# Performance work log

Measured on AMD Instinct MI355X. Metric: run time of the kernel, lower is better.

The kernel has to match this reference:

```python
import jax, jax.numpy as jnp
import numpy as np

K = 3            # context window size
VOCAB = 50257
EMBED = 1024
SEQ = 2048
BATCH = 2


def setup_inputs() -> dict:
    key = jax.random.key(0)
    ks = jax.random.split(key, 8)
    tokens_seq = jax.random.randint(ks[0], (SEQ, BATCH), 0, VOCAB, dtype=jnp.int64)
    s = 0.02
    E = jax.random.normal(ks[1], (VOCAB, EMBED), dtype=jnp.float32) * s
    W1 = jax.random.normal(ks[2], (K * EMBED, EMBED), dtype=jnp.float32) * s
    b1 = jnp.zeros((EMBED,), dtype=jnp.float32)
    W2 = jax.random.normal(ks[3], (EMBED, EMBED), dtype=jnp.float32) * s
    b2 = jnp.zeros((EMBED,), dtype=jnp.float32)
    Wout = jax.random.normal(ks[4], (EMBED, VOCAB), dtype=jnp.float32) * s
    bout = jnp.zeros((VOCAB,), dtype=jnp.float32)
    return {"tokens_seq": tokens_seq, "E": E, "W1": W1, "b1": b1,
            "W2": W2, "b2": b2, "Wout": Wout, "bout": bout}


def reference(tokens_seq, E, W1, b1, W2, b2, Wout, bout):
    S, B = tokens_seq.shape
    # pad with k-1 zero-token rows at the front, then take length-k windows
    pad = jnp.zeros((K - 1, B), dtype=tokens_seq.dtype)
    padded = jnp.concatenate([pad, tokens_seq], axis=0)          # (S+K-1, B)
    # windows[t, b, i] = padded[t+i, b]  (same as torch unfold + permute)
    windows = jnp.stack([padded[i:i + S] for i in range(K)], axis=-1)  # (S, B, K)
    emb = E[windows]                                              # (S, B, K, EMBED)
    x = emb.reshape(S, B, K * EMBED)                              # concat of k embeddings
    h = jax.nn.silu(jnp.einsum('sbi,io->sbo', x, W1) + b1)
    h = jax.nn.silu(jnp.einsum('sbi,io->sbo', h, W2) + b2)
    logits = jnp.einsum('sbi,iv->sbv', h, Wout) + bout            # (S, B, VOCAB)
    return logits
```

## Files before the change

kernel.cpp:

```cpp
#include <hip/hip_runtime.h>
#include <hip/hip_bf16.h>

#define SEQ    2048
#define BATCH  2
#define MROWS  (SEQ*BATCH)
#define EMBED  1024
#define KCTX   3
#define XDIM   (KCTX*EMBED)
#define VOCAB  50257
#define VPAD2  50432
#define GK     1024
#define NBLKN  197
#define NWG    (16*NBLKN)

using u16 = unsigned short;
typedef __attribute__((ext_vector_type(8))) short   frag_ab;
typedef __attribute__((ext_vector_type(4))) float   frag_cd;

__device__ __forceinline__ u16 f2bf(float f) {
  union { float f; unsigned u; } v; v.f = f;
  unsigned r = v.u + 0x7fffu + ((v.u >> 16) & 1u);
  return (u16)(r >> 16);
}

__device__ __forceinline__ void gload16(const u16* g, const u16* l) {
  __builtin_amdgcn_global_load_lds((const __attribute__((address_space(1))) void*)g,
                                   (__attribute__((address_space(3))) void*)l, 16, 0, 0);
}

__global__ void gather_x(const int* __restrict__ tokens,
                         const float* __restrict__ E,
                         u16* __restrict__ XB) {
  const int r = blockIdx.x;
  const int s = r >> 1, b = r & 1;
  #pragma unroll
  for (int i = 0; i < KCTX; ++i) {
    int t = s + i - (KCTX - 1);
    int tok = (t >= 0) ? tokens[t * BATCH + b] : 0;
    const float* src = &E[(size_t)tok * EMBED];
    u16* dst = &XB[(size_t)r * XDIM + i * EMBED];
    int c = threadIdx.x * 4;
    float4 v = *(const float4*)&src[c];
    u16 o[4] = { f2bf(v.x), f2bf(v.y), f2bf(v.z), f2bf(v.w) };
    *(ulong1*)&dst[c] = *(ulong1*)o;
  }
}

__global__ void transpose_cvt(const float* __restrict__ W,
                              u16* __restrict__ WT,
                              int K, int N) {
  __shared__ float tile[32][33];
  const int nb = blockIdx.x * 32, kb = blockIdx.y * 32;
  const int tx = threadIdx.x & 31, ty = threadIdx.x >> 5;
  #pragma unroll
  for (int i = 0; i < 32; i += 8) {
    int k = kb + ty + i, n = nb + tx;
    tile[ty + i][tx] = (n < N) ? W[(size_t)k * N + n] : 0.f;
  }
  __syncthreads();
  #pragma unroll
  for (int i = 0; i < 32; i += 8) {
    int n = nb + ty + i, k = kb + tx;
    WT[(size_t)n * K + k] = f2bf(tile[tx][ty + i]);
  }
}

template<int EPI>
__global__ __launch_bounds__(256, 2)
void gemm_bt(const u16* __restrict__ A, const u16* __restrict__ BT,
             const float* __restrict__ bias, void* __restrict__ Cout,
             int K, int Nout) {
  __shared__ u16 lA[128 * 64];
  __shared__ u16 lB[128 * 64];
  const int tid  = threadIdx.x;
  const int wave = tid >> 6, lane = tid & 63;
  const int m0 = blockIdx.y * 128;
  const int n0 = blockIdx.x * 128;
  const int wm = (wave >> 1) * 64;
  const int wn = (wave & 1) * 64;

  frag_cd acc[4][4];
  #pragma unroll
  for (int i = 0; i < 4; ++i)
    #pragma unroll
    for (int j = 0; j < 4; ++j)
      acc[i][j] = (frag_cd)0.f;

  const int srow = lane >> 3;
  const int skc  = ((lane & 7) ^ srow) * 8;

  for (int k0 = 0; k0 < K; k0 += 64) {
    #pragma unroll
    for (int i = 0; i < 4; ++i) {
      int chunk = wave * 4 + i;
      int r = chunk * 8 + srow;
      const u16* ga = &A [(size_t)(m0 + r) * K + k0 + skc];
      const u16* gb = &BT[(size_t)(n0 + r) * K + k0 + skc];
      gload16(ga, &lA[chunk * 512 + lane * 8]);
      gload16(gb, &lB[chunk * 512 + lane * 8]);
    }
    __syncthreads();

    #pragma unroll
    for (int kk = 0; kk < 2; ++kk) {
      const int c15 = lane & 15;
      const int s   = kk * 4 + (lane >> 4);
      const int ko  = (s ^ (c15 & 7)) * 8;
      frag_ab af[4], bfr[4];
      #pragma unroll
      for (int i = 0; i < 4; ++i) {
        af[i]  = *(const frag_ab*)&lA[(wm + i * 16 + c15) * 64 + ko];
        bfr[i] = *(const frag_ab*)&lB[(wn + i * 16 + c15) * 64 + ko];
      }
      #pragma unroll
      for (int i = 0; i < 4; ++i)
        #pragma unroll
        for (int j = 0; j < 4; ++j)
          acc[i][j] = __builtin_amdgcn_mfma_f32_16x16x32_bf16(
              af[i], bfr[j], acc[i][j], 0, 0, 0);
    }
    __syncthreads();
  }

  const int cr = (lane >> 4) * 4;
  const int cc = lane & 15;
  if (EPI == 0) {
    u16* H = (u16*)Cout;
    #pragma unroll
    for (int j = 0; j < 4; ++j) {
      int colg = n0 + wn + j * 16 + cc;
      float bv = bias[colg];
      #pragma unroll
      for (int i = 0; i < 4; ++i)
        #pragma unroll
        for (int t = 0; t < 4; ++t) {
          int rowg = m0 + wm + i * 16 + cr + t;
          float v = acc[i][j][t] + bv;
          v = v / (1.f + __expf(-v));
          H[(size_t)rowg * Nout + colg] = f2bf(v);
        }
    }
  } else {
    float* O = (float*)Cout;
    #pragma unroll
    for (int j = 0; j < 4; ++j) {
      int colg = n0 + wn + j * 16 + cc;
      if (colg < Nout) {
        float bv = bias[colg];
        #pragma unroll
        for (int i = 0; i < 4; ++i)
          #pragma unroll
          for (int t = 0; t < 4; ++t) {
            int rowg = m0 + wm + i * 16 + cr + t;
            O[(size_t)rowg * Nout + colg] = acc[i][j][t] + bv;
          }
      }
    }
  }
}

#define BARR   asm volatile("s_barrier" ::: "memory")
#define VMCNT4 asm volatile("s_waitcnt vmcnt(4)" ::: "memory")
#define LGKM0  asm volatile("s_waitcnt lgkmcnt(0)" ::: "memory")
#define SCHED0 __builtin_amdgcn_sched_barrier(0)
#define PRIO1  __builtin_amdgcn_s_setprio(1)
#define PRIO0  __builtin_amdgcn_s_setprio(0)

#define DSREAD(DST, AREG, IMM) \
  asm volatile("ds_read_b128 %0, %1 offset:%2" : "=v"(DST) : "v"(AREG), "i"(IMM))

#define ADV { pa0 += 32; pa1 += 32; pb0 += 32; pb1 += 32; }

#define KT(REGH, REGW, HIMM, WIMM, WP) { \
  VMCNT4; BARR; \
  gload16(pa0, (const u16*)(smraw + (WP)         + stoff)); \
  gload16(pa1, (const u16*)(smraw + (WP) +  8192 + stoff)); \
  gload16(pb0, (const u16*)(smraw + (WP) + 16384 + stoff)); \
  gload16(pb1, (const u16*)(smraw + (WP) + 24576 + stoff)); \
  ADV; \
  DSREAD(wF[0], REGW, (WIMM) + 0*1024); \
  DSREAD(wF[1], REGW, (WIMM) + 1*1024); \
  DSREAD(wF[2], REGW, (WIMM) + 2*1024); \
  DSREAD(wF[3], REGW, (WIMM) + 3*1024); \
  DSREAD(hF[0], REGH, (HIMM) + 0*1024); \
  DSREAD(hF[1], REGH, (HIMM) + 1*1024); \
  DSREAD(hF[2], REGH, (HIMM) + 2*1024); \
  DSREAD(hF[3], REGH, (HIMM) + 3*1024); \
  DSREAD(hF[4], REGH, (HIMM) + 4*1024); \
  DSREAD(hF[5], REGH, (HIMM) + 5*1024); \
  DSREAD(hF[6], REGH, (HIMM) + 6*1024); \
  DSREAD(hF[7], REGH, (HIMM) + 7*1024); \
  LGKM0; SCHED0; \
  PRIO1; \
  _Pragma("unroll") for (int nf = 0; nf < 4; ++nf) \
  _Pragma("unroll") for (int mf = 0; mf < 8; ++mf) \
    acc[mf][nf] = __builtin_amdgcn_mfma_f32_16x16x32_bf16(hF[mf], wF[nf], acc[mf][nf], 0, 0, 0); \
  PRIO0; SCHED0; }

__global__ __launch_bounds__(512, 2)
void gemm256(const u16* __restrict__ A, const u16* __restrict__ BT,
             const float* __restrict__ bias, float* __restrict__ O) {
  extern __shared__ char smraw[];

  const int bid = blockIdx.x;
  const int wg  = (bid & 7) * (NWG / 8) + (bid >> 3);
  const int m0  = (wg & 15) * 256;
  const int n0  = (wg >> 4) * 256;

  const int tid  = threadIdx.x;
  const int lane = tid & 63, wave = tid >> 6;
  const int wm = wave >> 2, wn = wave & 3;

  const int stoff = wave * 1024 + lane * 16;
  const int srow  = wave * 16 + (lane >> 2);
  const int ke    = ((lane & 3) ^ ((lane >> 3) & 3)) * 8;

  const u16* pa0 = A + (size_t)(m0 + srow      ) * GK + ke;
  const u16* pa1 = A + (size_t)(m0 + srow + 128) * GK + ke;
  const u16* pb0 = BT + (size_t)(n0 + srow      ) * GK + ke;
  const u16* pb1 = BT + (size_t)(n0 + srow + 128) * GK + ke;

  const unsigned dynbase = (unsigned)(size_t)(__attribute__((address_space(3))) char*)smraw;
  const int c = lane & 15, q = lane >> 4;
  const unsigned swq  = ((unsigned)q << 4) ^ (((unsigned)(c >> 1) & 3u) << 4);
  const unsigned regH_lo = dynbase + (unsigned)((wm * 128 + c) * 64) + swq;
  const unsigned regW_lo = dynbase + 16384u + (unsigned)((wn * 64 + c) * 64) + swq;
  const unsigned regH_hi = regH_lo + 65536u;
  const unsigned regW_hi = regW_lo + 65536u;

  frag_ab hF[8], wF[4];
  frag_cd acc[8][4];
  #pragma unroll
  for (int i = 0; i < 8; ++i)
    #pragma unroll
    for (int j = 0; j < 4; ++j)
      acc[i][j] = (frag_cd)0.f;

  gload16(pa0, (const u16*)(smraw +     0 + stoff));
  gload16(pa1, (const u16*)(smraw +  8192 + stoff));
  gload16(pb0, (const u16*)(smraw + 16384 + stoff));
  gload16(pb1, (const u16*)(smraw + 24576 + stoff));
  ADV;
  gload16(pa0, (const u16*)(smraw + 32768 +     0 + stoff));
  gload16(pa1, (const u16*)(smraw + 32768 +  8192 + stoff));
  gload16(pb0, (const u16*)(smraw + 32768 + 16384 + stoff));
  gload16(pb1, (const u16*)(smraw + 32768 + 24576 + stoff));
  ADV;

  #pragma unroll 1
  for (int tt = 0; tt < 10; ++tt) {
    KT(regH_lo, regW_lo,     0,     0, 65536);
    KT(regH_lo, regW_lo, 32768, 32768,     0);
    KT(regH_hi, regW_hi,     0,     0, 32768);
  }
  KT(regH_lo, regW_lo,     0,     0, 65536);
  KT(regH_lo, regW_lo, 32768, 32768,     0);

  asm volatile("s_waitcnt vmcnt(0) lgkmcnt(0)" ::: "memory");
  BARR;

  float* lfs = (float*)smraw;
  const int colg = n0 + wn * 64 + c * 4;
  #pragma unroll
  for (int mf = 0; mf < 8; ++mf) {
    const int lbase = wave * 1088 + (mf & 1) * 8704;
    #pragma unroll
    for (int nf = 0; nf < 4; ++nf)
      #pragma unroll
      for (int t = 0; t < 4; ++t)
        lfs[lbase + (q * 4 + t) * 68 + nf * 16 + c] = acc[mf][nf][t];
    #pragma unroll
    for (int p = 0; p < 4; ++p) {
      frag_cd v = *(const frag_cd*)&lfs[lbase + (p * 4 + q) * 68 + c * 4];
      const int rowg = m0 + wm * 128 + mf * 16 + p * 4 + q;
      if (colg + 3 < VOCAB) {
        frag_cd bv = *(const frag_cd*)&bias[colg];
        v += bv;
        *(frag_cd*)&O[(size_t)rowg * VOCAB + colg] = v;
      } else {
        #pragma unroll
        for (int t = 0; t < 4; ++t)
          if (colg + t < VOCAB)
            O[(size_t)rowg * VOCAB + colg + t] = v[t] + bias[colg + t];
      }
    }
  }
}

extern "C" void kernel_launch(void* const* d_in, const int* in_sizes, int n_in,
                              void* d_out, int out_size, void* d_ws, size_t ws_size,
                              hipStream_t stream) {
  const int*   tokens = (const int*)  d_in[0];
  const float* E      = (const float*)d_in[1];
  const float* W1     = (const float*)d_in[2];
  const float* b1     = (const float*)d_in[3];
  const float* W2     = (const float*)d_in[4];
  const float* b2     = (const float*)d_in[5];
  const float* Wout   = (const float*)d_in[6];
  const float* bout   = (const float*)d_in[7];
  float* out = (float*)d_out;

  char* p = (char*)d_ws;
  u16* XB  = (u16*)p; p += (size_t)MROWS * XDIM  * 2;
  u16* WOT = (u16*)p; p += (size_t)VPAD2 * EMBED * 2;
  u16* H1  = (u16*)p; p += (size_t)MROWS * EMBED * 2;
  u16* H2  = (u16*)p; p += (size_t)MROWS * EMBED * 2;
  u16* W1T = (u16*)p; p += (size_t)EMBED * XDIM  * 2;
  u16* W2T = (u16*)p; p += (size_t)EMBED * EMBED * 2;

  hipFuncSetAttribute((const void*)gemm256,
                      hipFuncAttributeMaxDynamicSharedMemorySize, 98304);

  gather_x<<<MROWS, 256, 0, stream>>>(tokens, E, XB);
  transpose_cvt<<<dim3(EMBED/32, XDIM/32),  256, 0, stream>>>(W1,   W1T, XDIM,  EMBED);
  transpose_cvt<<<dim3(EMBED/32, EMBED/32), 256, 0, stream>>>(W2,   W2T, EMBED, EMBED);
  transpose_cvt<<<dim3(VPAD2/32, EMBED/32), 256, 0, stream>>>(Wout, WOT, EMBED, VOCAB);

  gemm_bt<0><<<dim3(EMBED/128, MROWS/128), 256, 0, stream>>>(XB, W1T, b1, H1, XDIM,  EMBED);
  gemm_bt<0><<<dim3(EMBED/128, MROWS/128), 256, 0, stream>>>(H1, W2T, b2, H2, EMBED, EMBED);

  gemm256<<<NWG, 512, 98304, stream>>>(H2, WOT, bout, out);
}
```

Baseline: 796.5 us.

## Restructure vocab GEMM to BK=64 double-buffered pipeline with interleaved LDS waits

The output-projection GEMM changes from a triple-buffered K=32 pipeline to a double-buffered K=64 one, using 64 KB LDS stages, a new XOR swizzle and a reworked global-to-LDS load mapping. Each window waits for all outstanding global loads, issues the next stage's prefetch, then runs two 32-wide K halves. Within each half, MFMAs are split into per-row groups gated by decreasing lgkmcnt waits, so compute can start before every LDS read has returned. The aim is fewer barriers and better overlap of ds_reads with MFMA. The cost is a full vmcnt(0) wait per window, only one stage of prefetch lookahead, and a larger LDS footprint of 128 KB.

```diff
diff --git a/kernel.cpp b/kernel.cpp
--- a/kernel.cpp
+++ b/kernel.cpp
@@ -160,46 +160,65 @@
 }
 
 #define BARR   asm volatile("s_barrier" ::: "memory")
-#define VMCNT4 asm volatile("s_waitcnt vmcnt(4)" ::: "memory")
-#define LGKM0  asm volatile("s_waitcnt lgkmcnt(0)" ::: "memory")
+#define VMCNT0 asm volatile("s_waitcnt vmcnt(0)" ::: "memory")
+#define LGKMC(N) asm volatile("s_waitcnt lgkmcnt(" #N ")" ::: "memory")
 #define SCHED0 __builtin_amdgcn_sched_barrier(0)
 #define PRIO1  __builtin_amdgcn_s_setprio(1)
 #define PRIO0  __builtin_amdgcn_s_setprio(0)
-
 #define DSREAD(DST, AREG, IMM) \
   asm volatile("ds_read_b128 %0, %1 offset:%2" : "=v"(DST) : "v"(AREG), "i"(IMM))
-
-#define ADV { pa0 += 32; pa1 += 32; pb0 += 32; pb1 += 32; }
-
-#define KT(REGH, REGW, HIMM, WIMM, WP) { \
-  VMCNT4; BARR; \
-  gload16(pa0, (const u16*)(smraw + (WP)         + stoff)); \
-  gload16(pa1, (const u16*)(smraw + (WP) +  8192 + stoff)); \
-  gload16(pb0, (const u16*)(smraw + (WP) + 16384 + stoff)); \
-  gload16(pb1, (const u16*)(smraw + (WP) + 24576 + stoff)); \
-  ADV; \
-  DSREAD(wF[0], REGW, (WIMM) + 0*1024); \
-  DSREAD(wF[1], REGW, (WIMM) + 1*1024); \
-  DSREAD(wF[2], REGW, (WIMM) + 2*1024); \
-  DSREAD(wF[3], REGW, (WIMM) + 3*1024); \
-  DSREAD(hF[0], REGH, (HIMM) + 0*1024); \
-  DSREAD(hF[1], REGH, (HIMM) + 1*1024); \
-  DSREAD(hF[2], REGH, (HIMM) + 2*1024); \
-  DSREAD(hF[3], REGH, (HIMM) + 3*1024); \
-  DSREAD(hF[4], REGH, (HIMM) + 4*1024); \
-  DSREAD(hF[5], REGH, (HIMM) + 5*1024); \
-  DSREAD(hF[6], REGH, (HIMM) + 6*1024); \
-  DSREAD(hF[7], REGH, (HIMM) + 7*1024); \
-  LGKM0; SCHED0; \
+#define MFMA4(MF) { \
+  _Pragma("unroll") for (int nf = 0; nf < 4; ++nf) \
+    acc[MF][nf] = __builtin_amdgcn_mfma_f32_16x16x32_bf16(hF[MF], wF[nf], acc[MF][nf], 0, 0, 0); }
+
+#define BSTAGE(WP) { \
+  gload16(pa,          (const u16*)(smraw + (WP)         + stoffB)); \
+  gload16(pa +  65536, (const u16*)(smraw + (WP) +  8192 + stoffB)); \
+  gload16(pa + 131072, (const u16*)(smraw + (WP) + 16384 + stoffB)); \
+  gload16(pa + 196608, (const u16*)(smraw + (WP) + 24576 + stoffB)); \
+  gload16(pb,          (const u16*)(smraw + (WP) + 32768 + stoffB)); \
+  gload16(pb +  65536, (const u16*)(smraw + (WP) + 40960 + stoffB)); \
+  gload16(pb + 131072, (const u16*)(smraw + (WP) + 49152 + stoffB)); \
+  gload16(pb + 196608, (const u16*)(smraw + (WP) + 57344 + stoffB)); \
+  pa += 64; pb += 64; }
+
+#define BRD(REGW, REGH) { \
+  DSREAD(wF[0], REGW, 0*2048); \
+  DSREAD(wF[1], REGW, 1*2048); \
+  DSREAD(wF[2], REGW, 2*2048); \
+  DSREAD(wF[3], REGW, 3*2048); \
+  DSREAD(hF[0], REGH, 0*2048); \
+  DSREAD(hF[1], REGH, 1*2048); \
+  DSREAD(hF[2], REGH, 2*2048); \
+  DSREAD(hF[3], REGH, 3*2048); \
+  DSREAD(hF[4], REGH, 4*2048); \
+  DSREAD(hF[5], REGH, 5*2048); \
+  DSREAD(hF[6], REGH, 6*2048); \
+  DSREAD(hF[7], REGH, 7*2048); }
+
+#define GROUPS8 { \
   PRIO1; \
-  _Pragma("unroll") for (int nf = 0; nf < 4; ++nf) \
-  _Pragma("unroll") for (int mf = 0; mf < 8; ++mf) \
-    acc[mf][nf] = __builtin_amdgcn_mfma_f32_16x16x32_bf16(hF[mf], wF[nf], acc[mf][nf], 0, 0, 0); \
+  LGKMC(7); SCHED0; MFMA4(0); \
+  LGKMC(6); SCHED0; MFMA4(1); \
+  LGKMC(5); SCHED0; MFMA4(2); \
+  LGKMC(4); SCHED0; MFMA4(3); \
+  LGKMC(3); SCHED0; MFMA4(4); \
+  LGKMC(2); SCHED0; MFMA4(5); \
+  LGKMC(1); SCHED0; MFMA4(6); \
+  LGKMC(0); SCHED0; MFMA4(7); \
   PRIO0; SCHED0; }
 
+#define BWIN(RW0, RH0, RW1, RH1, WP) { \
+  VMCNT0; BARR; \
+  BSTAGE(WP); \
+  BRD(RW0, RH0); \
+  GROUPS8; \
+  BRD(RW1, RH1); \
+  GROUPS8; }
+
 __global__ __launch_bounds__(512, 2)
-void gemm256(const u16* __restrict__ A, const u16* __restrict__ BT,
-             const float* __restrict__ bias, float* __restrict__ O) {
+void gemm_bk64(const u16* __restrict__ A, const u16* __restrict__ BT,
+               const float* __restrict__ bias, float* __restrict__ O) {
   extern __shared__ char smraw[];
 
   const int bid = blockIdx.x;
@@ -211,22 +230,24 @@
   const int lane = tid & 63, wave = tid >> 6;
   const int wm = wave >> 2, wn = wave & 3;
 
-  const int stoff = wave * 1024 + lane * 16;
-  const int srow  = wave * 16 + (lane >> 2);
-  const int ke    = ((lane & 3) ^ ((lane >> 3) & 3)) * 8;
-
-  const u16* pa0 = A + (size_t)(m0 + srow      ) * GK + ke;
-  const u16* pa1 = A + (size_t)(m0 + srow + 128) * GK + ke;
-  const u16* pb0 = BT + (size_t)(n0 + srow      ) * GK + ke;
-  const u16* pb1 = BT + (size_t)(n0 + srow + 128) * GK + ke;
+  const int stoffB = tid * 16;
+  const int r8 = tid >> 3, slot = tid & 7;
+  const int ke = ((slot ^ (r8 & 7)) * 8);
+  const u16* pa = A  + (size_t)(m0 + r8) * GK + ke;
+  const u16* pb = BT + (size_t)(n0 + r8) * GK + ke;
 
   const unsigned dynbase = (unsigned)(size_t)(__attribute__((address_space(3))) char*)smraw;
   const int c = lane & 15, q = lane >> 4;
-  const unsigned swq  = ((unsigned)q << 4) ^ (((unsigned)(c >> 1) & 3u) << 4);
-  const unsigned regH_lo = dynbase + (unsigned)((wm * 128 + c) * 64) + swq;
-  const unsigned regW_lo = dynbase + 16384u + (unsigned)((wn * 64 + c) * 64) + swq;
-  const unsigned regH_hi = regH_lo + 65536u;
-  const unsigned regW_hi = regW_lo + 65536u;
+  const unsigned sw0 = (unsigned)(((q    ) ^ (c & 7)) * 16);
+  const unsigned sw1 = (unsigned)(((q + 4) ^ (c & 7)) * 16);
+  const unsigned regH_h0_p0 = dynbase + (unsigned)((wm * 128 + c) * 128) + sw0;
+  const unsigned regH_h1_p0 = dynbase + (unsigned)((wm * 128 + c) * 128) + sw1;
+  const unsigned regW_h0_p0 = dynbase + 32768u + (unsigned)((wn * 64 + c) * 128) + sw0;
+  const unsigned regW_h1_p0 = dynbase + 32768u + (unsigned)((wn * 64 + c) * 128) + sw1;
+  const unsigned regH_h0_p1 = regH_h0_p0 + 65536u;
+  const unsigned regH_h1_p1 = regH_h1_p0 + 65536u;
+  const unsigned regW_h0_p1 = regW_h0_p0 + 65536u;
+  const unsigned regW_h1_p1 = regW_h1_p0 + 65536u;
 
   frag_ab hF[8], wF[4];
   frag_cd acc[8][4];
@@ -236,25 +257,13 @@
     for (int j = 0; j < 4; ++j)
       acc[i][j] = (frag_cd)0.f;
 
-  gload16(pa0, (const u16*)(smraw +     0 + stoff));
-  gload16(pa1, (const u16*)(smraw +  8192 + stoff));
-  gload16(pb0, (const u16*)(smraw + 16384 + stoff));
-  gload16(pb1, (const u16*)(smraw + 24576 + stoff));
-  ADV;
-  gload16(pa0, (const u16*)(smraw + 32768 +     0 + stoff));
-  gload16(pa1, (const u16*)(smraw + 32768 +  8192 + stoff));
-  gload16(pb0, (const u16*)(smraw + 32768 + 16384 + stoff));
-  gload16(pb1, (const u16*)(smraw + 32768 + 24576 + stoff));
-  ADV;
+  BSTAGE(0);
 
   #pragma unroll 1
-  for (int tt = 0; tt < 10; ++tt) {
-    KT(regH_lo, regW_lo,     0,     0, 65536);
-    KT(regH_lo, regW_lo, 32768, 32768,     0);
-    KT(regH_hi, regW_hi,     0,     0, 32768);
-  }
-  KT(regH_lo, regW_lo,     0,     0, 65536);
-  KT(regH_lo, regW_lo, 32768, 32768,     0);
+  for (int w = 0; w < 8; ++w) {
+    BWIN(regW_h0_p0, regH_h0_p0, regW_h1_p0, regH_h1_p0, 65536);
+    BWIN(regW_h0_p1, regH_h0_p1, regW_h1_p1, regH_h1_p1, 0);
+  }
 
   asm volatile("s_waitcnt vmcnt(0) lgkmcnt(0)" ::: "memory");
   BARR;
@@ -308,8 +317,8 @@
   u16* W1T = (u16*)p; p += (size_t)EMBED * XDIM  * 2;
   u16* W2T = (u16*)p; p += (size_t)EMBED * EMBED * 2;
 
-  hipFuncSetAttribute((const void*)gemm256,
-                      hipFuncAttributeMaxDynamicSharedMemorySize, 98304);
+  hipFuncSetAttribute((const void*)gemm_bk64,
+                      hipFuncAttributeMaxDynamicSharedMemorySize, 131072);
 
   gather_x<<<MROWS, 256, 0, stream>>>(tokens, E, XB);
   transpose_cvt<<<dim3(EMBED/32, XDIM/32),  256, 0, stream>>>(W1,   W1T, XDIM,  EMBED);
@@ -319,5 +328,5 @@
   gemm_bt<0><<<dim3(EMBED/128, MROWS/128), 256, 0, stream>>>(XB, W1T, b1, H1, XDIM,  EMBED);
   gemm_bt<0><<<dim3(EMBED/128, MROWS/128), 256, 0, stream>>>(H1, W2T, b2, H2, EMBED, EMBED);
 
-  gemm256<<<NWG, 512, 98304, stream>>>(H2, WOT, bout, out);
-}
+  gemm_bk64<<<NWG, 512, 131072, stream>>>(H2, WOT, bout, out);
+}
```

Measured after the change: 772.6 us. 3.0% less time.
